# Kernel optimization log

Hardware: AMD Instinct MI355X
Metric: run time of the kernel (lower is better)

## Reference

```python
import jax, jax.numpy as jnp
import numpy as np

NUM_POINTS = 7
SCALES = (0.25, 0.125, 0.0625, 0.03125)
LENS_AREA = (8, 25)
OUTPUT_SIZES = ((8, 32), (8, 64))
CANON_SCALE = 224.0  # LevelMapper defaults (ctor's 160 is not forwarded)
CANON_LVL = 4.0
K_MIN, K_MAX = 2.0, 5.0
EPS = 1e-6


def _boundary_interp(pts, wp):
    # pts: [N, n, 2] polyline; sample wp points uniformly in arc parameter
    n = pts.shape[1]
    u = (jnp.arange(wp, dtype=pts.dtype) + 0.5) / wp * (n - 1)
    i0 = jnp.clip(jnp.floor(u).astype(jnp.int32), 0, n - 2)
    f = (u - i0.astype(pts.dtype))[None, :, None]
    return pts[:, i0] * (1 - f) + pts[:, i0 + 1] * f  # [N, wp, 2]


def _make_grid(polys_norm, hp, wp):
    # polys_norm: [N, 2n, 2] normalized to [0,1]; first n = top l->r, last n = bottom l->r
    n = polys_norm.shape[1] // 2
    top = _boundary_interp(polys_norm[:, :n], wp)
    bot = _boundary_interp(polys_norm[:, n:], wp)
    v = ((jnp.arange(hp, dtype=polys_norm.dtype) + 0.5) / hp)[None, :, None, None]
    return top[:, None] * (1 - v) + bot[:, None] * v  # [N, hp, wp, 2] (x,y)


def _bilinear(feat, img_ids, grid):
    # feat [B,C,H,W]; grid normalized [0,1] image coords -> pixel coords of this level
    B, C, H, W = feat.shape
    x = grid[..., 0] * W - 0.5
    y = grid[..., 1] * H - 0.5
    x0 = jnp.floor(x)
    y0 = jnp.floor(y)
    wx = (x - x0)[..., None]
    wy = (y - y0)[..., None]
    x0i = x0.astype(jnp.int32)
    y0i = y0.astype(jnp.int32)
    ids = img_ids[:, None, None]

    def g(xi, yi):
        xc = jnp.clip(xi, 0, W - 1)
        yc = jnp.clip(yi, 0, H - 1)
        val = feat[ids, :, yc, xc]  # [N, hp, wp, C]
        m = ((xi >= 0) & (xi < W) & (yi >= 0) & (yi < H))[..., None]
        return val * m.astype(feat.dtype)

    out = (g(x0i, y0i) * (1 - wx) * (1 - wy)
           + g(x0i + 1, y0i) * wx * (1 - wy)
           + g(x0i, y0i + 1) * (1 - wx) * wy
           + g(x0i + 1, y0i + 1) * wx * wy)
    return jnp.transpose(out, (0, 3, 1, 2))  # [N, C, hp, wp]


def _forward(feats, polys, img_ids, lens):
    n = NUM_POINTS
    idx = list(range(n)) + list(range(n, 2 * n))[::-1]  # top l->r, bottom flipped l->r
    H0, W0 = feats[0].shape[-2:]
    wh = jnp.array([W0 / SCALES[0], H0 / SCALES[0]], dtype=feats[0].dtype)
    polys_norm = polys[:, idx] / wh
    # FPN level routing from bbox area of the polygon (boxlist.area heuristic)
    s = jnp.sqrt((polys[..., 0].max(1) - polys[..., 0].min(1))
                 * (polys[..., 1].max(1) - polys[..., 1].min(1)))
    lvl = jnp.clip(jnp.floor(CANON_LVL + jnp.log2(s / CANON_SCALE + EPS)),
                   K_MIN, K_MAX).astype(jnp.int32) - int(K_MIN)
    # text-length bucket -> pooler id (first bucket whose len_max >= len)
    thr = jnp.array(LENS_AREA[:-1], dtype=lens.dtype)
    pooler_id = jnp.sum(lens[:, None] > thr[None, :], axis=1).astype(jnp.int32)

    outs = []
    N, C = polys.shape[0], feats[0].shape[1]
    for pid, (hp, wp) in enumerate(OUTPUT_SIZES):
        grid = _make_grid(polys_norm, hp, wp)
        acc = jnp.zeros((N, C, hp, wp), feats[0].dtype)
        for l, f in enumerate(feats):
            sel = ((lvl == l) & (pooler_id == pid))[:, None, None, None]
            acc = jnp.where(sel, _bilinear(f, img_ids, grid), acc)
        outs.append(acc)
    return tuple(outs)


def setup_inputs() -> dict:
    B, C, H0, W0 = 2, 256, 200, 336
    N, n = 256, NUM_POINTS
    key = jax.random.key(0)
    k0, k1, k2, k3 = jax.random.split(key, 4)
    feat0 = jax.random.normal(k0, (B, C, H0, W0), jnp.float32)
    feat1 = jax.random.normal(k1, (B, C, H0 // 2, W0 // 2), jnp.float32)
    feat2 = jax.random.normal(k2, (B, C, H0 // 4, W0 // 4), jnp.float32)
    feat3 = jax.random.normal(k3, (B, C, H0 // 8, W0 // 8), jnp.float32)
    rng = np.random.default_rng(0)
    img_w, img_h = W0 / SCALES[0], H0 / SCALES[0]
    cx = rng.uniform(0.25, 0.75, N) * img_w
    cy = rng.uniform(0.2, 0.8, N) * img_h
    w = rng.uniform(40.0, 600.0, N)
    h = rng.uniform(16.0, 80.0, N)
    t = np.linspace(0.0, 1.0, n)
    top_x = cx[:, None] + (t[None, :] - 0.5) * w[:, None]
    top_y = cy[:, None] - h[:, None] / 2 + rng.uniform(-2, 2, (N, n))
    bot_y = cy[:, None] + h[:, None] / 2 + rng.uniform(-2, 2, (N, n))
    # stored polygon order: top l->r then bottom r->l (matches self.idx reorder)
    top = np.stack([top_x, top_y], -1)
    bot = np.stack([top_x[:, ::-1], bot_y[:, ::-1]], -1)
    polys = jnp.asarray(np.concatenate([top, bot], 1), jnp.float32)  # [N, 14, 2]
    img_ids = jnp.asarray(rng.integers(0, B, N), jnp.int32)
    lens = jnp.asarray(rng.integers(1, 25, N), jnp.int32)
    return {"feat0": feat0, "feat1": feat1, "feat2": feat2, "feat3": feat3,
            "polys": polys, "img_ids": img_ids, "lens": lens}


def reference(feat0, feat1, feat2, feat3, polys, img_ids, lens):
    return _forward((feat0, feat1, feat2, feat3), polys, img_ids, lens)
```

## Files before the change

kernel.cpp:

```cpp
#include <hip/hip_runtime.h>


#define NBOX 256
#define NCH  256
#define HP   8
#define CCHUNK 32
#define NSTG 4
#define PMAX 1280
#define OUT0_ELEMS ((size_t)NBOX * NCH * HP * 32)

typedef float f32x4 __attribute__((ext_vector_type(4)));

__device__ __forceinline__ void make_geo(
    const float* __restrict__ pts, int pos, int lwp, int W, int H,
    int pxo, int pyo, int PWe,
    int& o00, int& o10, int& o01, int& o11,
    float& w00, float& w10, float& w01, float& w11)
{
    const int wp = 1 << lwp;
    const int i  = pos >> lwp;
    const int j  = pos & (wp - 1);

    float u  = ((j + 0.5f) / (float)wp) * 6.0f;
    int   i0 = (int)floorf(u);
    i0 = min(max(i0, 0), 5);
    float f = u - (float)i0;

    float txa = pts[2 * i0]     / 1344.0f, tya = pts[2 * i0 + 1] / 800.0f;
    float txb = pts[2 * i0 + 2] / 1344.0f, tyb = pts[2 * i0 + 3] / 800.0f;
    int ka = 13 - i0, kb = 12 - i0;
    float bxa = pts[2 * ka] / 1344.0f, bya = pts[2 * ka + 1] / 800.0f;
    float bxb = pts[2 * kb] / 1344.0f, byb = pts[2 * kb + 1] / 800.0f;

    float topx = txa * (1.0f - f) + txb * f;
    float topy = tya * (1.0f - f) + tyb * f;
    float botx = bxa * (1.0f - f) + bxb * f;
    float boty = bya * (1.0f - f) + byb * f;

    float v  = (i + 0.5f) / 8.0f;
    float gx = topx * (1.0f - v) + botx * v;
    float gy = topy * (1.0f - v) + boty * v;

    float x = gx * (float)W - 0.5f;
    float y = gy * (float)H - 0.5f;
    float x0f = floorf(x), y0f = floorf(y);
    float fx = x - x0f,   fy = y - y0f;
    int x0 = (int)x0f, y0 = (int)y0f;
    int x1 = x0 + 1,   y1 = y0 + 1;

    int x0c = min(max(x0, 0), W - 1), x1c = min(max(x1, 0), W - 1);
    int y0c = min(max(y0, 0), H - 1), y1c = min(max(y1, 0), H - 1);
    float m00 = (x0 >= 0 && x0 < W && y0 >= 0 && y0 < H) ? 1.0f : 0.0f;
    float m10 = (x1 >= 0 && x1 < W && y0 >= 0 && y0 < H) ? 1.0f : 0.0f;
    float m01 = (x0 >= 0 && x0 < W && y1 >= 0 && y1 < H) ? 1.0f : 0.0f;
    float m11 = (x1 >= 0 && x1 < W && y1 >= 0 && y1 < H) ? 1.0f : 0.0f;

    o00 = (y0c - pyo) * PWe + (x0c - pxo);
    o10 = (y0c - pyo) * PWe + (x1c - pxo);
    o01 = (y1c - pyo) * PWe + (x0c - pxo);
    o11 = (y1c - pyo) * PWe + (x1c - pxo);
    w00 = (1.0f - fx) * (1.0f - fy) * m00;
    w10 = fx * (1.0f - fy) * m10;
    w01 = (1.0f - fx) * fy * m01;
    w11 = fx * fy * m11;
}

__global__ __launch_bounds__(256) void poly_pool_kernel(
    const float* __restrict__ f0, const float* __restrict__ f1,
    const float* __restrict__ f2, const float* __restrict__ f3,
    const float* __restrict__ polys, const int* __restrict__ img_ids,
    const int* __restrict__ lens, float* __restrict__ out)
{
    const int b    = blockIdx.y;
    const int pidk = blockIdx.z;
    const int lwp  = 5 + pidk;
    const int npos = HP << lwp;
    const int c0   = blockIdx.x * CCHUNK;
    const int tid  = threadIdx.x;

    float* outb = out + (pidk ? OUT0_ELEMS : (size_t)0) + (size_t)b * NCH * npos;

    const int pooler = (lens[b] > 8) ? 1 : 0;
    if (pooler != pidk) {
        f32x4 z = (f32x4)(0.0f);
        f32x4* p = reinterpret_cast<f32x4*>(outb + (size_t)c0 * npos);
        const int total4 = (CCHUNK * npos) >> 2;
        for (int k = tid; k < total4; k += 256) p[k] = z;
        return;
    }

    __shared__ float pts[28];
    __shared__ float patch[NSTG][PMAX];
    if (tid < 28) pts[tid] = polys[b * 28 + tid];
    __syncthreads();

    float minx = pts[0], maxx = pts[0], miny = pts[1], maxy = pts[1];
#pragma unroll
    for (int k = 1; k < 14; ++k) {
        float x = pts[2 * k], y = pts[2 * k + 1];
        minx = fminf(minx, x); maxx = fmaxf(maxx, x);
        miny = fminf(miny, y); maxy = fmaxf(maxy, y);
    }
    float s = sqrtf((maxx - minx) * (maxy - miny));
    int lvl = (int)floorf(4.0f + log2f(s / 224.0f + 1e-6f));
    lvl = min(max(lvl, 2), 5) - 2;

    const float* feat; int H, W;
    switch (lvl) {
        case 0:  feat = f0; H = 200; W = 336; break;
        case 1:  feat = f1; H = 100; W = 168; break;
        case 2:  feat = f2; H = 50;  W = 84;  break;
        default: feat = f3; H = 25;  W = 42;  break;
    }
    const int img = img_ids[b];
    const int HW  = H * W;
    const float* featimg = feat + (size_t)img * NCH * HW;

    float sxn = (float)W / 1344.0f, syn = (float)H / 800.0f;
    int px0 = min(max((int)floorf(minx * sxn - 0.5f), 0), W - 1);
    int px1 = min(max((int)floorf(maxx * sxn - 0.5f) + 1, 0), W - 1);
    int py0 = min(max((int)floorf(miny * syn - 0.5f), 0), H - 1);
    int py1 = min(max((int)floorf(maxy * syn - 0.5f) + 1, 0), H - 1);
    const int PW = px1 - px0 + 1;
    const int PH = py1 - py0 + 1;
    const int npatch = PH * PW;
    const bool staged = (PW <= 256) && (npatch <= PMAX);

    const int pxo = staged ? px0 : 0;
    const int pyo = staged ? py0 : 0;
    const int PWe = staged ? PW  : W;

    const int pg   = tid & ((npos >> 2) - 1);
    const int csub = tid >> (lwp + 1);
    const int npass = pidk ? 2 : 1;

    int   off[4][4];
    float wt [4][4];
#pragma unroll
    for (int k = 0; k < 4; ++k)
        make_geo(pts, 4 * pg + k, lwp, W, H, pxo, pyo, PWe,
                 off[k][0], off[k][1], off[k][2], off[k][3],
                 wt[k][0],  wt[k][1],  wt[k][2],  wt[k][3]);

    if (staged) {
        for (int rnd = 0; rnd < CCHUNK / NSTG; ++rnd) {
            const float* sb = featimg + (size_t)(c0 + rnd * NSTG) * HW
                              + (size_t)py0 * W + px0;
            for (int r = 0; r < PH; r += 2) {
                if (tid < PW) {
                    const float* sA = sb + r * W + tid;
                    float a0 = sA[0], a1 = sA[HW], a2 = sA[2 * HW], a3 = sA[3 * HW];
                    const bool r1 = (r + 1 < PH);
                    const float* sB = sA + W;
                    float b0 = 0, b1 = 0, b2 = 0, b3 = 0;
                    if (r1) { b0 = sB[0]; b1 = sB[HW]; b2 = sB[2 * HW]; b3 = sB[3 * HW]; }
                    int d = r * PW + tid;
                    patch[0][d] = a0; patch[1][d] = a1;
                    patch[2][d] = a2; patch[3][d] = a3;
                    if (r1) {
                        int d2 = d + PW;
                        patch[0][d2] = b0; patch[1][d2] = b1;
                        patch[2][d2] = b2; patch[3][d2] = b3;
                    }
                }
            }
            __syncthreads();

            for (int cc = 0; cc < npass; ++cc) {
                const int slot = (cc << 1) + csub;
                const float* pk = patch[slot];
                f32x4 res;
#pragma unroll
                for (int k = 0; k < 4; ++k)
                    res[k] = wt[k][0] * pk[off[k][0]] + wt[k][1] * pk[off[k][1]]
                           + wt[k][2] * pk[off[k][2]] + wt[k][3] * pk[off[k][3]];
                const int ch = c0 + (rnd << 2) + slot;
                *reinterpret_cast<f32x4*>(outb + (size_t)ch * npos + (pg << 2)) = res;
            }
            __syncthreads();
        }
    } else {
        for (int rnd = 0; rnd < CCHUNK / NSTG; ++rnd) {
            for (int cc = 0; cc < npass; ++cc) {
                const int slot = (cc << 1) + csub;
                const int ch = c0 + (rnd << 2) + slot;
                const float* fc = featimg + (size_t)ch * HW;
                f32x4 res;
#pragma unroll
                for (int k = 0; k < 4; ++k)
                    res[k] = wt[k][0] * fc[off[k][0]] + wt[k][1] * fc[off[k][1]]
                           + wt[k][2] * fc[off[k][2]] + wt[k][3] * fc[off[k][3]];
                *reinterpret_cast<f32x4*>(outb + (size_t)ch * npos + (pg << 2)) = res;
            }
        }
    }
}

extern "C" void kernel_launch(void* const* d_in, const int* in_sizes, int n_in,
                              void* d_out, int out_size, void* d_ws, size_t ws_size,
                              hipStream_t stream) {
    const float* f0    = (const float*)d_in[0];
    const float* f1    = (const float*)d_in[1];
    const float* f2    = (const float*)d_in[2];
    const float* f3    = (const float*)d_in[3];
    const float* polys = (const float*)d_in[4];
    const int*   ids   = (const int*)d_in[5];
    const int*   lens  = (const int*)d_in[6];
    float* out = (float*)d_out;

    dim3 grid(NCH / CCHUNK, NBOX, 2);
    poly_pool_kernel<<<grid, 256, 0, stream>>>(f0, f1, f2, f3, polys, ids, lens, out);
}
```

Measured before the change: 397.0 us.

## Register-prefetch next channel patch, pad patch rows, nontemporal stores, flatten grid

Patch staging is restructured so all 256 threads load the patch into registers over a power-of-two padded row layout. The next round's channel slab is prefetched while the current one is being interpolated, replacing the old loop where only PW threads loaded rows serially. Output and zero-fill stores become nontemporal, and the 3D grid is flattened to 1D with box as the fastest index. The cost is higher register pressure from the prefetch arrays and a larger LDS buffer, which may reduce occupancy.

```diff
diff --git a/kernel.cpp b/kernel.cpp
--- a/kernel.cpp
+++ b/kernel.cpp
@@ -3,19 +3,18 @@
 
 #define NBOX 256
 #define NCH  256
-#define HP   8
 #define CCHUNK 32
 #define NSTG 4
-#define PMAX 1280
-#define OUT0_ELEMS ((size_t)NBOX * NCH * HP * 32)
+#define PMAX 2560
+#define MAXIT 5
+#define OUT0_ELEMS ((size_t)NBOX * NCH * 8 * 32)
 
 typedef float f32x4 __attribute__((ext_vector_type(4)));
 
 __device__ __forceinline__ void make_geo(
     const float* __restrict__ pts, int pos, int lwp, int W, int H,
     int pxo, int pyo, int PWe,
-    int& o00, int& o10, int& o01, int& o11,
-    float& w00, float& w10, float& w01, float& w11)
+    int* __restrict__ off, float* __restrict__ wt)
 {
     const int wp = 1 << lwp;
     const int i  = pos >> lwp;
@@ -26,11 +25,12 @@
     i0 = min(max(i0, 0), 5);
     float f = u - (float)i0;
 
-    float txa = pts[2 * i0]     / 1344.0f, tya = pts[2 * i0 + 1] / 800.0f;
-    float txb = pts[2 * i0 + 2] / 1344.0f, tyb = pts[2 * i0 + 3] / 800.0f;
+    const float inx = 1.0f / 1344.0f, iny = 1.0f / 800.0f;
+    float txa = pts[2 * i0]     * inx, tya = pts[2 * i0 + 1] * iny;
+    float txb = pts[2 * i0 + 2] * inx, tyb = pts[2 * i0 + 3] * iny;
     int ka = 13 - i0, kb = 12 - i0;
-    float bxa = pts[2 * ka] / 1344.0f, bya = pts[2 * ka + 1] / 800.0f;
-    float bxb = pts[2 * kb] / 1344.0f, byb = pts[2 * kb + 1] / 800.0f;
+    float bxa = pts[2 * ka] * inx, bya = pts[2 * ka + 1] * iny;
+    float bxb = pts[2 * kb] * inx, byb = pts[2 * kb + 1] * iny;
 
     float topx = txa * (1.0f - f) + txb * f;
     float topy = tya * (1.0f - f) + tyb * f;
@@ -55,14 +55,14 @@
     float m01 = (x0 >= 0 && x0 < W && y1 >= 0 && y1 < H) ? 1.0f : 0.0f;
     float m11 = (x1 >= 0 && x1 < W && y1 >= 0 && y1 < H) ? 1.0f : 0.0f;
 
-    o00 = (y0c - pyo) * PWe + (x0c - pxo);
-    o10 = (y0c - pyo) * PWe + (x1c - pxo);
-    o01 = (y1c - pyo) * PWe + (x0c - pxo);
-    o11 = (y1c - pyo) * PWe + (x1c - pxo);
-    w00 = (1.0f - fx) * (1.0f - fy) * m00;
-    w10 = fx * (1.0f - fy) * m10;
-    w01 = (1.0f - fx) * fy * m01;
-    w11 = fx * fy * m11;
+    off[0] = (y0c - pyo) * PWe + (x0c - pxo);
+    off[1] = (y0c - pyo) * PWe + (x1c - pxo);
+    off[2] = (y1c - pyo) * PWe + (x0c - pxo);
+    off[3] = (y1c - pyo) * PWe + (x1c - pxo);
+    wt[0] = (1.0f - fx) * (1.0f - fy) * m00;
+    wt[1] = fx * (1.0f - fy) * m10;
+    wt[2] = (1.0f - fx) * fy * m01;
+    wt[3] = fx * fy * m11;
 }
 
 __global__ __launch_bounds__(256) void poly_pool_kernel(
@@ -71,11 +71,14 @@
     const float* __restrict__ polys, const int* __restrict__ img_ids,
     const int* __restrict__ lens, float* __restrict__ out)
 {
-    const int b    = blockIdx.y;
-    const int pidk = blockIdx.z;
+    const int n    = blockIdx.x;
+    const int b    = n & (NBOX - 1);
+    const int slab = n >> 8;
+    const int cxb  = slab & 7;
+    const int pidk = slab >> 3;
     const int lwp  = 5 + pidk;
-    const int npos = HP << lwp;
-    const int c0   = blockIdx.x * CCHUNK;
+    const int npos = 8 << lwp;
+    const int c0   = cxb * CCHUNK;
     const int tid  = threadIdx.x;
 
     float* outb = out + (pidk ? OUT0_ELEMS : (size_t)0) + (size_t)b * NCH * npos;
@@ -85,7 +88,8 @@
         f32x4 z = (f32x4)(0.0f);
         f32x4* p = reinterpret_cast<f32x4*>(outb + (size_t)c0 * npos);
         const int total4 = (CCHUNK * npos) >> 2;
-        for (int k = tid; k < total4; k += 256) p[k] = z;
+        for (int k = tid; k < total4; k += 256)
+            __builtin_nontemporal_store(z, p + k);
         return;
     }
 
@@ -112,9 +116,8 @@
         case 2:  feat = f2; H = 50;  W = 84;  break;
         default: feat = f3; H = 25;  W = 42;  break;
     }
-    const int img = img_ids[b];
-    const int HW  = H * W;
-    const float* featimg = feat + (size_t)img * NCH * HW;
+    const int HW = H * W;
+    const float* featimg = feat + (size_t)img_ids[b] * NCH * HW;
 
     float sxn = (float)W / 1344.0f, syn = (float)H / 800.0f;
     int px0 = min(max((int)floorf(minx * sxn - 0.5f), 0), W - 1);
@@ -123,74 +126,99 @@
     int py1 = min(max((int)floorf(maxy * syn - 0.5f) + 1, 0), H - 1);
     const int PW = px1 - px0 + 1;
     const int PH = py1 - py0 + 1;
-    const int npatch = PH * PW;
+    const int lg = (PW <= 64) ? 6 : ((PW <= 128) ? 7 : 8);
+    const int PWP = 1 << lg;
+    const int npatch = PH << lg;
     const bool staged = (PW <= 256) && (npatch <= PMAX);
 
     const int pxo = staged ? px0 : 0;
     const int pyo = staged ? py0 : 0;
-    const int PWe = staged ? PW  : W;
-
-    const int pg   = tid & ((npos >> 2) - 1);
-    const int csub = tid >> (lwp + 1);
-    const int npass = pidk ? 2 : 1;
+    const int PWe = staged ? PWP : W;
+
+    const int groups = npos >> 2;
+    const int pg     = tid & (groups - 1);
+    const int csub   = tid / groups;
+    const int npass  = pidk ? 2 : 1;
 
     int   off[4][4];
     float wt [4][4];
 #pragma unroll
     for (int k = 0; k < 4; ++k)
-        make_geo(pts, 4 * pg + k, lwp, W, H, pxo, pyo, PWe,
-                 off[k][0], off[k][1], off[k][2], off[k][3],
-                 wt[k][0],  wt[k][1],  wt[k][2],  wt[k][3]);
+        make_geo(pts, 4 * pg + k, lwp, W, H, pxo, pyo, PWe, off[k], wt[k]);
+
+    float* opb = outb + 4 * pg;
 
     if (staged) {
+        float pfa[MAXIT][NSTG], pfb[MAXIT][NSTG];
+
+#define PREFETCH(RR)                                                          \
+        { const float* sb = featimg + (size_t)(c0 + (RR) * NSTG) * HW         \
+                            + (size_t)py0 * W + px0;                          \
+          _Pragma("unroll")                                                   \
+          for (int it = 0; it < MAXIT; ++it) {                                \
+              int e = tid + it * 512;                                         \
+              if (e < npatch) {                                               \
+                  int eb = min(e + 256, npatch - 1);                          \
+                  int ra = e  >> lg, ca = min(e  & (PWP - 1), PW - 1);        \
+                  int rb = eb >> lg, cb = min(eb & (PWP - 1), PW - 1);        \
+                  const float* sA = sb + ra * W + ca;                         \
+                  const float* sB = sb + rb * W + cb;                         \
+                  pfa[it][0] = sA[0];      pfa[it][1] = sA[HW];               \
+                  pfa[it][2] = sA[2 * HW]; pfa[it][3] = sA[3 * HW];           \
+                  pfb[it][0] = sB[0];      pfb[it][1] = sB[HW];               \
+                  pfb[it][2] = sB[2 * HW]; pfb[it][3] = sB[3 * HW];           \
+              } } }
+
+#define WRITELDS                                                              \
+        { _Pragma("unroll")                                                   \
+          for (int it = 0; it < MAXIT; ++it) {                                \
+              int e = tid + it * 512;                                         \
+              if (e < npatch) {                                               \
+                  int eb = min(e + 256, npatch - 1);                          \
+                  patch[0][e]  = pfa[it][0]; patch[1][e]  = pfa[it][1];       \
+                  patch[2][e]  = pfa[it][2]; patch[3][e]  = pfa[it][3];       \
+                  patch[0][eb] = pfb[it][0]; patch[1][eb] = pfb[it][1];       \
+                  patch[2][eb] = pfb[it][2]; patch[3][eb] = pfb[it][3];       \
+              } } }
+
+        PREFETCH(0);
+        WRITELDS;
+        __syncthreads();
+
         for (int rnd = 0; rnd < CCHUNK / NSTG; ++rnd) {
-            const float* sb = featimg + (size_t)(c0 + rnd * NSTG) * HW
-                              + (size_t)py0 * W + px0;
-            for (int r = 0; r < PH; r += 2) {
-                if (tid < PW) {
-                    const float* sA = sb + r * W + tid;
-                    float a0 = sA[0], a1 = sA[HW], a2 = sA[2 * HW], a3 = sA[3 * HW];
-                    const bool r1 = (r + 1 < PH);
-                    const float* sB = sA + W;
-                    float b0 = 0, b1 = 0, b2 = 0, b3 = 0;
-                    if (r1) { b0 = sB[0]; b1 = sB[HW]; b2 = sB[2 * HW]; b3 = sB[3 * HW]; }
-                    int d = r * PW + tid;
-                    patch[0][d] = a0; patch[1][d] = a1;
-                    patch[2][d] = a2; patch[3][d] = a3;
-                    if (r1) {
-                        int d2 = d + PW;
-                        patch[0][d2] = b0; patch[1][d2] = b1;
-                        patch[2][d2] = b2; patch[3][d2] = b3;
-                    }
-                }
-            }
-            __syncthreads();
+            if (rnd + 1 < CCHUNK / NSTG) PREFETCH(rnd + 1);
 
             for (int cc = 0; cc < npass; ++cc) {
-                const int slot = (cc << 1) + csub;
+                const int slot = pidk ? ((cc << 1) + csub) : csub;
                 const float* pk = patch[slot];
                 f32x4 res;
 #pragma unroll
                 for (int k = 0; k < 4; ++k)
                     res[k] = wt[k][0] * pk[off[k][0]] + wt[k][1] * pk[off[k][1]]
                            + wt[k][2] * pk[off[k][2]] + wt[k][3] * pk[off[k][3]];
-                const int ch = c0 + (rnd << 2) + slot;
-                *reinterpret_cast<f32x4*>(outb + (size_t)ch * npos + (pg << 2)) = res;
+                const int ch = c0 + rnd * NSTG + slot;
+                __builtin_nontemporal_store(res,
+                    reinterpret_cast<f32x4*>(opb + (size_t)ch * npos));
             }
             __syncthreads();
+            if (rnd + 1 < CCHUNK / NSTG) {
+                WRITELDS;
+                __syncthreads();
+            }
         }
     } else {
         for (int rnd = 0; rnd < CCHUNK / NSTG; ++rnd) {
             for (int cc = 0; cc < npass; ++cc) {
-                const int slot = (cc << 1) + csub;
-                const int ch = c0 + (rnd << 2) + slot;
+                const int slot = pidk ? ((cc << 1) + csub) : csub;
+                const int ch = c0 + rnd * NSTG + slot;
                 const float* fc = featimg + (size_t)ch * HW;
                 f32x4 res;
 #pragma unroll
                 for (int k = 0; k < 4; ++k)
                     res[k] = wt[k][0] * fc[off[k][0]] + wt[k][1] * fc[off[k][1]]
                            + wt[k][2] * fc[off[k][2]] + wt[k][3] * fc[off[k][3]];
-                *reinterpret_cast<f32x4*>(outb + (size_t)ch * npos + (pg << 2)) = res;
+                __builtin_nontemporal_store(res,
+                    reinterpret_cast<f32x4*>(opb + (size_t)ch * npos));
             }
         }
     }
@@ -208,6 +236,6 @@
     const int*   lens  = (const int*)d_in[6];
     float* out = (float*)d_out;
 
-    dim3 grid(NCH / CCHUNK, NBOX, 2);
-    poly_pool_kernel<<<grid, 256, 0, stream>>>(f0, f1, f2, f3, polys, ids, lens, out);
+    poly_pool_kernel<<<dim3(4096), 256, 0, stream>>>(f0, f1, f2, f3,
+                                                     polys, ids, lens, out);
 }
```

Result: faster. 373.9 us (-5.8%).
